# Kernel optimization log

Hardware: AMD Instinct MI355X
Metric: run time of the kernel (lower is better)

## Reference

```python
import jax, jax.numpy as jnp
import numpy as np

N_NODES = 100000
N_EDGES = 3200000


def setup_inputs() -> dict:
    key = jax.random.key(0)
    ks = jax.random.split(key, 12)
    inp = {
        "x": jax.random.normal(ks[0], (N_NODES, 4), dtype=jnp.float32),
        "edge": jax.random.randint(ks[1], (2, N_EDGES), 0, N_NODES, dtype=jnp.int64),
        "weight": jax.random.uniform(ks[2], (N_EDGES,), dtype=jnp.float32),
        "W1": jax.random.normal(ks[3], (8, 4), dtype=jnp.float32) * 0.5,
        "b1": jax.random.normal(ks[4], (8,), dtype=jnp.float32) * 0.1,
        "W3": jax.random.normal(ks[5], (16, 8), dtype=jnp.float32) * 0.35,
        "b3": jax.random.normal(ks[6], (16,), dtype=jnp.float32) * 0.1,
        "W5": jax.random.normal(ks[7], (32, 16), dtype=jnp.float32) * 0.25,
        "b5": jax.random.normal(ks[8], (32,), dtype=jnp.float32) * 0.1,
        "W7": jax.random.normal(ks[9], (2, 32), dtype=jnp.float32) * 0.18,
        "b7": jax.random.normal(ks[10], (2,), dtype=jnp.float32) * 0.1,
    }
    return inp


def reference(x, edge, weight, W1, b1, W3, b3, W5, b5, W7, b7):
    row, col = edge[0], edge[1]
    n = x.shape[0]
    lrelu = jax.nn.leaky_relu  # default negative_slope=0.01, same as torch
    # per-row edge counts for scatter_mean (rows with 0 edges -> 0, like torch_scatter)
    cnt = jax.ops.segment_sum(jnp.ones_like(weight), row, num_segments=n)
    inv_cnt = jnp.where(cnt > 0, 1.0 / jnp.maximum(cnt, 1.0), 0.0)[:, None]

    def block(h, W, b):
        msg = h[col] * weight[:, None]          # gather + edge-weight scale [E,F]
        msg = lrelu(msg @ W.T + b)              # per-edge Linear + LeakyReLU
        agg = jax.ops.segment_sum(msg, row, num_segments=n) * inv_cnt  # scatter_mean
        return agg + lrelu(h @ W.T + b)         # residual branch

    h = block(x, W1, b1)   # [N,8]
    h = block(h, W3, b3)   # [N,16]
    h = block(h, W5, b5)   # [N,32]
    pooled = jnp.mean(h, axis=0, keepdims=True)  # global_mean_pool (single graph) [1,32]
    logits = pooled @ W7.T + b7                  # [1,2]
    return jax.nn.log_softmax(logits, axis=1)
```

## Files before the change

### kernel.cpp

```cpp
#include <hip/hip_runtime.h>
#include <hip/hip_bf16.h>
#include <math.h>

#define LB256 __launch_bounds__(256)

#define NB_SHIFT 8
#define NB_ROWS  (1 << NB_SHIFT)
#define GA 512

template <int PT>
__global__ LB256 void gscan_sum(const int* __restrict__ a, int n, int* __restrict__ bsum) {
    int base = blockIdx.x * (256 * PT);
    int sum = 0;
    for (int i = threadIdx.x; i < 256 * PT; i += 256) {
        int idx = base + i;
        sum += (idx < n) ? a[idx] : 0;
    }
#pragma unroll
    for (int o = 32; o; o >>= 1) sum += __shfl_down(sum, o);
    __shared__ int ws[4];
    if ((threadIdx.x & 63) == 0) ws[threadIdx.x >> 6] = sum;
    __syncthreads();
    if (threadIdx.x == 0) bsum[blockIdx.x] = ws[0] + ws[1] + ws[2] + ws[3];
}

__global__ void gscan_offsets(const int* __restrict__ bsum, int nbk, int* __restrict__ boff) {
    int lane = threadIdx.x;
    int v = (lane < nbk) ? bsum[lane] : 0;
    int orig = v;
#pragma unroll
    for (int o = 1; o < 64; o <<= 1) {
        int u = __shfl_up(v, o);
        if (lane >= o) v += u;
    }
    if (lane < nbk) boff[lane] = v - orig;
}

template <int PT>
__global__ LB256 void gscan_scatter(const int* __restrict__ a, int n,
                                    const int* __restrict__ boff, int total,
                                    int* __restrict__ out1) {
    int base = blockIdx.x * (256 * PT);
    int idx0 = base + threadIdx.x * PT;
    int vals[PT];
    int s = 0;
#pragma unroll
    for (int k = 0; k < PT; ++k) {
        int id = idx0 + k;
        vals[k] = (id < n) ? a[id] : 0;
        s += vals[k];
    }
    int lane = threadIdx.x & 63, wid = threadIdx.x >> 6;
    int inc = s;
#pragma unroll
    for (int o = 1; o < 64; o <<= 1) {
        int u = __shfl_up(inc, o);
        if (lane >= o) inc += u;
    }
    __shared__ int wsum[4];
    if (lane == 63) wsum[wid] = inc;
    __syncthreads();
    int woff = 0;
    for (int i = 0; i < wid; ++i) woff += wsum[i];
    int excl = inc - s + woff + boff[blockIdx.x];
#pragma unroll
    for (int k = 0; k < PT; ++k) {
        int id = idx0 + k;
        if (id < n) out1[id] = excl;
        excl += vals[k];
    }
    if (blockIdx.x == 0 && threadIdx.x == 0) out1[n] = total;
}


__global__ LB256 void hist_kernel(const int* __restrict__ row, int E, int nb, int chunk,
                                  int* __restrict__ countmat) {
    __shared__ int lh[512];
    for (int b = threadIdx.x; b < nb; b += 256) lh[b] = 0;
    __syncthreads();
    int beg = blockIdx.x * chunk;
    int end = min(E, beg + chunk);
    for (int i = beg + threadIdx.x; i < end; i += 256)
        atomicAdd(&lh[row[i] >> NB_SHIFT], 1);
    __syncthreads();
    for (int b = threadIdx.x; b < nb; b += 256)
        countmat[b * gridDim.x + blockIdx.x] = lh[b];
}

__global__ LB256 void bucket_scatter_kernel(const int* __restrict__ row, const int* __restrict__ col,
                                            const float* __restrict__ w, const int* __restrict__ off,
                                            int E, int nb, int chunk,
                                            unsigned* __restrict__ tmpA,
                                            unsigned char* __restrict__ tmpB) {
    __shared__ int lc[512];
    __shared__ int loff[512];
    for (int b = threadIdx.x; b < nb; b += 256) {
        lc[b] = 0;
        loff[b] = off[b * gridDim.x + blockIdx.x];
    }
    __syncthreads();
    int beg = blockIdx.x * chunk;
    int end = min(E, beg + chunk);
    for (int i = beg + threadIdx.x; i < end; i += 256) {
        int r = row[i];
        int b = r >> NB_SHIFT;
        int lpos = atomicAdd(&lc[b], 1);
        unsigned wb = (__float_as_uint(w[i]) + 0x8000u) >> 16;
        int pos = loff[b] + lpos;
        tmpA[pos] = (wb << 17) | (unsigned)col[i];
        tmpB[pos] = (unsigned char)(r & (NB_ROWS - 1));
    }
}

__global__ LB256 void csr_build_kernel(const unsigned* __restrict__ tmpA,
                                       const unsigned char* __restrict__ tmpB,
                                       const int* __restrict__ off,
                                       int G, int N, int E,
                                       int* __restrict__ rowptr, unsigned* __restrict__ csr) {
    __shared__ int lcnt[NB_ROWS];
    __shared__ int wsum[4];
    int b = blockIdx.x;
    int tid = threadIdx.x;
    int s0 = off[b * G];
    int e0 = off[(b + 1) * G];
    int rbase = b << NB_SHIFT;

    lcnt[tid] = 0;
    __syncthreads();
    for (int j = s0 + tid; j < e0; j += 256)
        atomicAdd(&lcnt[tmpB[j]], 1);
    __syncthreads();

    int val = lcnt[tid];
    int lane = tid & 63, wid = tid >> 6;
    int inc = val;
#pragma unroll
    for (int o = 1; o < 64; o <<= 1) {
        int u = __shfl_up(inc, o);
        if (lane >= o) inc += u;
    }
    if (lane == 63) wsum[wid] = inc;
    __syncthreads();
    int woff = 0;
    for (int i = 0; i < wid; ++i) woff += wsum[i];
    int ex = inc - val + woff;

    int idx = rbase + tid;
    if (idx < N) rowptr[idx] = s0 + ex;
    if (b == gridDim.x - 1 && tid == 0) rowptr[N] = E;
    __syncthreads();
    lcnt[tid] = ex;
    __syncthreads();

    for (int j = s0 + tid; j < e0; j += 256) {
        unsigned a = tmpA[j];
        int pos = s0 + atomicAdd(&lcnt[tmpB[j]], 1);
        csr[pos] = a;
    }
}


template <int FIN, int FOUT>
__global__ LB256 void transform_kernel(const float* __restrict__ h, const float* __restrict__ W,
                                       __hip_bfloat16* __restrict__ t0,
                                       __hip_bfloat16* __restrict__ t1, int n) {
    constexpr int FH = (FOUT > 16) ? 16 : FOUT;
    int i = blockIdx.x * blockDim.x + threadIdx.x;
    if (i >= n * FOUT) return;
    int v = i / FOUT;
    int f = i % FOUT;
    float s = 0.0f;
#pragma unroll
    for (int k = 0; k < FIN; ++k) s = fmaf(h[v * FIN + k], W[f * FIN + k], s);
    __hip_bfloat16 bv = __float2bfloat16(s);
    if (f < FH) t0[v * FH + f] = bv;
    else        t1[v * FH + (f - FH)] = bv;
}

template <int GS, int FTOT>
__global__ LB256 void agg_half_kernel(const int* __restrict__ rowptr,
                                      const unsigned* __restrict__ csr,
                                      const unsigned* __restrict__ th,
                                      const float* __restrict__ b, int fo,
                                      float* __restrict__ h, int N) {
    constexpr int RPB = 256 / GS;
    int g = threadIdx.x / GS;
    int l = threadIdx.x % GS;
    int v = blockIdx.x * RPB + g;
    if (v >= N) return;
    int beg = rowptr[v], end = rowptr[v + 1];
    float bf0 = b[fo + 2 * l];
    float bf1 = b[fo + 2 * l + 1];
    float a0 = 0.0f, a1 = 0.0f;

    int j = beg;
    for (; j + 7 < end; j += 8) {
        unsigned e[8];
#pragma unroll
        for (int u = 0; u < 8; ++u) e[u] = __builtin_nontemporal_load(&csr[j + u]);
        unsigned tv[8];
#pragma unroll
        for (int u = 0; u < 8; ++u) tv[u] = th[(e[u] & 0x1FFFFu) * GS + l];
#pragma unroll
        for (int u = 0; u < 8; ++u) {
            float wv = __uint_as_float((e[u] & 0xFFFE0000u) >> 1);
            float m0 = fmaf(wv, __uint_as_float(tv[u] << 16), bf0);
            float m1 = fmaf(wv, __uint_as_float(tv[u] & 0xffff0000u), bf1);
            a0 += (m0 > 0.f) ? m0 : 0.01f * m0;
            a1 += (m1 > 0.f) ? m1 : 0.01f * m1;
        }
    }
    for (; j < end; ++j) {
        unsigned e0 = __builtin_nontemporal_load(&csr[j]);
        unsigned t0 = th[(e0 & 0x1FFFFu) * GS + l];
        float wv = __uint_as_float((e0 & 0xFFFE0000u) >> 1);
        float m0 = fmaf(wv, __uint_as_float(t0 << 16), bf0);
        float m1 = fmaf(wv, __uint_as_float(t0 & 0xffff0000u), bf1);
        a0 += (m0 > 0.f) ? m0 : 0.01f * m0;
        a1 += (m1 > 0.f) ? m1 : 0.01f * m1;
    }

    int deg = end - beg;
    float iv = deg ? 1.0f / (float)deg : 0.0f;
    unsigned tr = th[v * GS + l];
    float r0 = __uint_as_float(tr << 16) + bf0;
    float r1 = __uint_as_float(tr & 0xffff0000u) + bf1;
    r0 = (r0 > 0.f) ? r0 : 0.01f * r0;
    r1 = (r1 > 0.f) ? r1 : 0.01f * r1;
    float2 st = make_float2(fmaf(a0, iv, r0), fmaf(a1, iv, r1));
    *(float2*)(h + (size_t)v * FTOT + fo + 2 * l) = st;
}


__global__ LB256 void pool_kernel(const float* __restrict__ h, float* __restrict__ pool, int n) {
    __shared__ float ls[256];
    int f = threadIdx.x & 31;
    int grp = threadIdx.x >> 5;
    int gid = blockIdx.x * (blockDim.x >> 5) + grp;
    int ngrp = (blockDim.x >> 5) * gridDim.x;
    float s = 0.0f;
    for (int v = gid; v < n; v += ngrp) s += h[v * 32 + f];
    ls[threadIdx.x] = s;
    __syncthreads();
    if (threadIdx.x < 32) {
        float tot = 0.0f;
#pragma unroll
        for (int g = 0; g < 8; ++g) tot += ls[g * 32 + threadIdx.x];
        atomicAdd(&pool[threadIdx.x], tot);
    }
}

__global__ void head_kernel(const float* __restrict__ pool, const float* __restrict__ W7,
                            const float* __restrict__ b7, float* __restrict__ out, int n) {
    if (threadIdx.x != 0 || blockIdx.x != 0) return;
    float invn = 1.0f / (float)n;
    float l0 = b7[0], l1 = b7[1];
    for (int f = 0; f < 32; ++f) {
        float p = pool[f] * invn;
        l0 = fmaf(p, W7[f], l0);
        l1 = fmaf(p, W7[32 + f], l1);
    }
    float m = fmaxf(l0, l1);
    float lse = m + logf(expf(l0 - m) + expf(l1 - m));
    out[0] = l0 - lse;
    out[1] = l1 - lse;
}


extern "C" void kernel_launch(void* const* d_in, const int* in_sizes, int n_in,
                              void* d_out, int out_size, void* d_ws, size_t ws_size,
                              hipStream_t stream) {
    const float* x  = (const float*)d_in[0];
    const int* edge = (const int*)d_in[1];
    const float* w  = (const float*)d_in[2];
    const float* W1 = (const float*)d_in[3];
    const float* b1 = (const float*)d_in[4];
    const float* W3 = (const float*)d_in[5];
    const float* b3 = (const float*)d_in[6];
    const float* W5 = (const float*)d_in[7];
    const float* b5 = (const float*)d_in[8];
    const float* W7 = (const float*)d_in[9];
    const float* b7 = (const float*)d_in[10];
    float* out = (float*)d_out;

    const int N = in_sizes[0] / 4;
    const int E = in_sizes[1] / 2;
    const int* row = edge;
    const int* col = edge + E;

    const int nb = (N + NB_ROWS - 1) >> NB_SHIFT;
    const int G = GA;
    const int chunk = (E + G - 1) / G;
    const int M = nb * G;

    char* ws = (char*)d_ws;
    size_t off8 = 0;
    auto alloc = [&](size_t bytes) {
        void* p = ws + off8;
        off8 += (bytes + 255) & ~(size_t)255;
        return p;
    };
    int*      bsum     = (int*)alloc(256 * 4);
    int*      boff     = (int*)alloc(256 * 4);
    int*      countmat = (int*)alloc((size_t)M * 4);
    int*      offm     = (int*)alloc(((size_t)M + 1) * 4);
    int*      rowptr   = (int*)alloc(((size_t)N + 1) * 4);
    float*    pool     = (float*)alloc(32 * 4);
    unsigned* csr      = (unsigned*)alloc((size_t)E * 4);
    __hip_bfloat16* t0 = (__hip_bfloat16*)alloc((size_t)N * 16 * 2);
    __hip_bfloat16* t1 = (__hip_bfloat16*)alloc((size_t)N * 16 * 2);
    float*    h1       = (float*)alloc((size_t)N * 8 * 4);
    float*    h2       = (float*)alloc((size_t)N * 16 * 4);
    size_t tmpsz = (size_t)E * 4 + 256 + (size_t)E;
    size_t h3sz  = (size_t)N * 32 * 4;
    char*  big   = (char*)alloc(tmpsz > h3sz ? tmpsz : h3sz);
    unsigned*      tmpA = (unsigned*)big;
    unsigned char* tmpB = (unsigned char*)(big + (((size_t)E * 4 + 255) & ~(size_t)255));
    float*         h3   = (float*)big;
    (void)ws_size;

    hipMemsetAsync(pool, 0, 32 * 4, stream);

    const int B = 256;
    const int nbkM = (M + 4095) / 4096;

    hist_kernel<<<G, B, 0, stream>>>(row, E, nb, chunk, countmat);
    gscan_sum<16><<<nbkM, B, 0, stream>>>(countmat, M, bsum);
    gscan_offsets<<<1, 64, 0, stream>>>(bsum, nbkM, boff);
    gscan_scatter<16><<<nbkM, B, 0, stream>>>(countmat, M, boff, E, offm);
    bucket_scatter_kernel<<<G, B, 0, stream>>>(row, col, w, offm, E, nb, chunk, tmpA, tmpB);
    csr_build_kernel<<<nb, B, 0, stream>>>(tmpA, tmpB, offm, G, N, E, rowptr, csr);

    transform_kernel<4, 8><<<(N * 8 + B - 1) / B, B, 0, stream>>>(x, W1, t0, t0, N);
    agg_half_kernel<4, 8><<<(N + 63) / 64, B, 0, stream>>>(rowptr, csr, (const unsigned*)t0, b1, 0, h1, N);

    transform_kernel<8, 16><<<(N * 16 + B - 1) / B, B, 0, stream>>>(h1, W3, t0, t0, N);
    agg_half_kernel<8, 16><<<(N + 31) / 32, B, 0, stream>>>(rowptr, csr, (const unsigned*)t0, b3, 0, h2, N);

    transform_kernel<16, 32><<<(N * 32 + B - 1) / B, B, 0, stream>>>(h2, W5, t0, t1, N);
    agg_half_kernel<8, 32><<<(N + 31) / 32, B, 0, stream>>>(rowptr, csr, (const unsigned*)t0, b5, 0, h3, N);
    agg_half_kernel<8, 32><<<(N + 31) / 32, B, 0, stream>>>(rowptr, csr, (const unsigned*)t1, b5, 16, h3, N);

    pool_kernel<<<256, B, 0, stream>>>(h3, pool, N);
    head_kernel<<<1, 64, 0, stream>>>(pool, W7, b7, out, N);
}
```

Measured before the change: 407.7 us.

## Locally sort edge tiles by bucket in LDS before scattering to global

Replaces the bucket scatter with a tile-local counting sort: each block stages 2048 edges in shared memory ordered by bucket, then writes them out so consecutive threads hit contiguous global runs. The packed row/col/weight entry becomes a single 64-bit word instead of a separate 32-bit array plus byte array. This aims to cut scattered, uncoalesced global writes in CSR construction, at the cost of extra LDS traffic, several block barriers per tile, and a wider temporary buffer.

```diff
diff --git a/kernel.cpp b/kernel.cpp
--- a/kernel.cpp
+++ b/kernel.cpp
@@ -7,6 +7,7 @@
 #define NB_SHIFT 8
 #define NB_ROWS  (1 << NB_SHIFT)
 #define GA 512
+#define TILE 2048
 
 template <int PT>
 __global__ LB256 void gscan_sum(const int* __restrict__ a, int n, int* __restrict__ bsum) {
@@ -76,7 +77,7 @@
 __global__ LB256 void hist_kernel(const int* __restrict__ row, int E, int nb, int chunk,
                                   int* __restrict__ countmat) {
     __shared__ int lh[512];
-    for (int b = threadIdx.x; b < nb; b += 256) lh[b] = 0;
+    for (int b = threadIdx.x; b < 512; b += 256) lh[b] = 0;
     __syncthreads();
     int beg = blockIdx.x * chunk;
     int end = min(E, beg + chunk);
@@ -87,33 +88,79 @@
         countmat[b * gridDim.x + blockIdx.x] = lh[b];
 }
 
-__global__ LB256 void bucket_scatter_kernel(const int* __restrict__ row, const int* __restrict__ col,
-                                            const float* __restrict__ w, const int* __restrict__ off,
-                                            int E, int nb, int chunk,
-                                            unsigned* __restrict__ tmpA,
-                                            unsigned char* __restrict__ tmpB) {
-    __shared__ int lc[512];
-    __shared__ int loff[512];
-    for (int b = threadIdx.x; b < nb; b += 256) {
-        lc[b] = 0;
-        loff[b] = off[b * gridDim.x + blockIdx.x];
-    }
-    __syncthreads();
-    int beg = blockIdx.x * chunk;
-    int end = min(E, beg + chunk);
-    for (int i = beg + threadIdx.x; i < end; i += 256) {
-        int r = row[i];
-        int b = r >> NB_SHIFT;
-        int lpos = atomicAdd(&lc[b], 1);
-        unsigned wb = (__float_as_uint(w[i]) + 0x8000u) >> 16;
-        int pos = loff[b] + lpos;
-        tmpA[pos] = (wb << 17) | (unsigned)col[i];
-        tmpB[pos] = (unsigned char)(r & (NB_ROWS - 1));
-    }
-}
-
-__global__ LB256 void csr_build_kernel(const unsigned* __restrict__ tmpA,
-                                       const unsigned char* __restrict__ tmpB,
+__global__ LB256 void sort_scatter_kernel(const int* __restrict__ row, const int* __restrict__ col,
+                                          const float* __restrict__ w, const int* __restrict__ off,
+                                          int E, int G, int chunk,
+                                          unsigned long long* __restrict__ tmp) {
+    __shared__ unsigned long long stage[TILE];
+    __shared__ int lh[512];
+    __shared__ int seg[512];
+    __shared__ int gcur[512];
+    __shared__ int wsum[4];
+    int blk = blockIdx.x, tid = threadIdx.x;
+    int beg = blk * chunk, end = min(E, beg + chunk);
+    for (int b = tid; b < 512; b += 256) {
+        gcur[b] = off[b * G + blk];
+        lh[b] = 0;
+    }
+    __syncthreads();
+
+    for (int tbase = beg; tbase < end; tbase += TILE) {
+        int tcnt = min(TILE, end - tbase);
+        int bk[8], sl[8];
+        unsigned long long en[8];
+#pragma unroll
+        for (int k = 0; k < 8; ++k) {
+            int e = tbase + k * 256 + tid;
+            bk[k] = -1;
+            if (e < end) {
+                int r = row[e];
+                int b = r >> NB_SHIFT;
+                unsigned wb = (__float_as_uint(w[e]) + 0x8000u) >> 16;
+                en[k] = ((unsigned long long)b << 40) |
+                        ((unsigned long long)(r & (NB_ROWS - 1)) << 32) |
+                        (unsigned long long)((wb << 17) | (unsigned)col[e]);
+                bk[k] = b;
+                sl[k] = atomicAdd(&lh[b], 1);
+            }
+        }
+        __syncthreads();
+        int c0 = lh[2 * tid], c1 = lh[2 * tid + 1];
+        int tsum = c0 + c1;
+        int lane = tid & 63, wid = tid >> 6;
+        int inc = tsum;
+#pragma unroll
+        for (int o = 1; o < 64; o <<= 1) {
+            int u = __shfl_up(inc, o);
+            if (lane >= o) inc += u;
+        }
+        if (lane == 63) wsum[wid] = inc;
+        __syncthreads();
+        int woff = 0;
+        for (int i = 0; i < wid; ++i) woff += wsum[i];
+        int ex = inc - tsum + woff;
+        seg[2 * tid] = ex;
+        seg[2 * tid + 1] = ex + c0;
+        __syncthreads();
+#pragma unroll
+        for (int k = 0; k < 8; ++k)
+            if (bk[k] >= 0) stage[seg[bk[k]] + sl[k]] = en[k];
+        __syncthreads();
+        for (int p = tid; p < tcnt; p += 256) {
+            unsigned long long ent = stage[p];
+            int b = (int)(ent >> 40);
+            tmp[gcur[b] + (p - seg[b])] = ent;
+        }
+        __syncthreads();
+        for (int b = tid; b < 512; b += 256) {
+            gcur[b] += lh[b];
+            lh[b] = 0;
+        }
+        __syncthreads();
+    }
+}
+
+__global__ LB256 void csr_build_kernel(const unsigned long long* __restrict__ tmp,
                                        const int* __restrict__ off,
                                        int G, int N, int E,
                                        int* __restrict__ rowptr, unsigned* __restrict__ csr) {
@@ -128,7 +175,7 @@
     lcnt[tid] = 0;
     __syncthreads();
     for (int j = s0 + tid; j < e0; j += 256)
-        atomicAdd(&lcnt[tmpB[j]], 1);
+        atomicAdd(&lcnt[(int)((tmp[j] >> 32) & 0xFFu)], 1);
     __syncthreads();
 
     int val = lcnt[tid];
@@ -153,9 +200,9 @@
     __syncthreads();
 
     for (int j = s0 + tid; j < e0; j += 256) {
-        unsigned a = tmpA[j];
-        int pos = s0 + atomicAdd(&lcnt[tmpB[j]], 1);
-        csr[pos] = a;
+        unsigned long long ent = tmp[j];
+        int pos = s0 + atomicAdd(&lcnt[(int)((ent >> 32) & 0xFFu)], 1);
+        csr[pos] = (unsigned)ent;
     }
 }
 
@@ -311,12 +358,11 @@
     __hip_bfloat16* t1 = (__hip_bfloat16*)alloc((size_t)N * 16 * 2);
     float*    h1       = (float*)alloc((size_t)N * 8 * 4);
     float*    h2       = (float*)alloc((size_t)N * 16 * 4);
-    size_t tmpsz = (size_t)E * 4 + 256 + (size_t)E;
+    size_t tmpsz = (size_t)E * 8;
     size_t h3sz  = (size_t)N * 32 * 4;
     char*  big   = (char*)alloc(tmpsz > h3sz ? tmpsz : h3sz);
-    unsigned*      tmpA = (unsigned*)big;
-    unsigned char* tmpB = (unsigned char*)(big + (((size_t)E * 4 + 255) & ~(size_t)255));
-    float*         h3   = (float*)big;
+    unsigned long long* tmp = (unsigned long long*)big;
+    float*              h3  = (float*)big;
     (void)ws_size;
 
     hipMemsetAsync(pool, 0, 32 * 4, stream);
@@ -328,8 +374,8 @@
     gscan_sum<16><<<nbkM, B, 0, stream>>>(countmat, M, bsum);
     gscan_offsets<<<1, 64, 0, stream>>>(bsum, nbkM, boff);
     gscan_scatter<16><<<nbkM, B, 0, stream>>>(countmat, M, boff, E, offm);
-    bucket_scatter_kernel<<<G, B, 0, stream>>>(row, col, w, offm, E, nb, chunk, tmpA, tmpB);
-    csr_build_kernel<<<nb, B, 0, stream>>>(tmpA, tmpB, offm, G, N, E, rowptr, csr);
+    sort_scatter_kernel<<<G, B, 0, stream>>>(row, col, w, offm, E, G, chunk, tmp);
+    csr_build_kernel<<<nb, B, 0, stream>>>(tmp, offm, G, N, E, rowptr, csr);
 
     transform_kernel<4, 8><<<(N * 8 + B - 1) / B, B, 0, stream>>>(x, W1, t0, t0, N);
     agg_half_kernel<4, 8><<<(N + 63) / 64, B, 0, stream>>>(rowptr, csr, (const unsigned*)t0, b1, 0, h1, N);
```

Result: faster. 366.9 us (-10.0%).
